# Kernel tuning notes

Hardware: AMD Instinct MI355X
Metric: run time of the kernel (lower is better)

Reference implementation:

```python
import jax, jax.numpy as jnp
import numpy as np

WINDOWP = 64
LN_EPS = 1e-5


def setup_inputs() -> dict:
    key = jax.random.key(0)
    ks = jax.random.split(key, 4)
    B, T, D = 8, 2048, 1024
    feature = jax.random.normal(ks[0], (B, T, D), dtype=jnp.float32)
    wq_w = jax.random.normal(ks[1], (D, D), dtype=jnp.float32) * 0.02  # x @ wq_w + wq_b
    wq_b = jnp.zeros((D,), dtype=jnp.float32)
    w2_w = jax.random.normal(ks[2], (D,), dtype=jnp.float32) * 0.02
    w2_b = jnp.zeros((1,), dtype=jnp.float32)
    ln_g = jnp.ones((D,), dtype=jnp.float32)
    ln_b = jnp.zeros((D,), dtype=jnp.float32)
    return {"feature": feature, "wq_w": wq_w, "wq_b": wq_b,
            "w2_w": w2_w, "w2_b": w2_b, "ln_g": ln_g, "ln_b": ln_b}


def _layer_norm(y, g, b):
    mu = jnp.mean(y, axis=-1, keepdims=True)
    var = jnp.mean((y - mu) ** 2, axis=-1, keepdims=True)
    return (y - mu) * jax.lax.rsqrt(var + LN_EPS) * g + b


def reference(feature, wq_w, wq_b, w2_w, w2_b, ln_g, ln_b):
    # feature: [B, T, D]
    B, T, D = feature.shape
    W = WINDOWP
    q_local = feature @ wq_w + wq_b  # [B, T, D]

    # First W positions: v_local[:, i] = feature[:, i]
    init_buf = feature[:, :W, :]  # sliding buffer of last W outputs, [B, W, D]

    def step(buf, q_i):
        # ki = v_local[:, i-W : i+1]; slot i is still zero when read (torch writes after)
        ki = jnp.concatenate([buf, jnp.zeros((B, 1, D), feature.dtype)], axis=1)  # [B, W+1, D]
        scores = jnp.einsum('bwd,d->bw', q_i[:, None, :] * ki, w2_w) + w2_b[0]  # [B, W+1]
        alpha = jax.nn.softmax(scores, axis=1)
        v_i = jnp.einsum('bwd,bw->bd', ki, alpha)  # [B, D]
        new_buf = jnp.concatenate([buf[:, 1:, :], v_i[:, None, :]], axis=1)
        return new_buf, v_i

    qs = jnp.transpose(q_local[:, W:, :], (1, 0, 2))  # [T-W, B, D]
    _, vs = jax.lax.scan(step, init_buf, qs)          # vs: [T-W, B, D]
    v_local = jnp.concatenate([feature[:, :W, :], jnp.transpose(vs, (1, 0, 2))], axis=1)

    y = jnp.tanh(v_local) * feature + feature
    return _layer_norm(y, ln_g, ln_b)
```

## Files before the change

### kernel.cpp

```cpp
#include <hip/hip_runtime.h>
#include <hip/hip_bf16.h>

#define B_ 8
#define T_ 2048
#define D_ 1024
#define W_ 64
#define LN_EPS 1e-5f
#define LOG2E 1.4426950408889634f

typedef __attribute__((ext_vector_type(8))) short bf16x8;
typedef __attribute__((ext_vector_type(4))) float f32x4;
typedef __attribute__((ext_vector_type(2))) float f32x2;
typedef unsigned short ushort_t;

__device__ __forceinline__ ushort_t f32_to_bf16(float f) {
    union { float ff; unsigned u; } c; c.ff = f;
    unsigned r = (c.u + 0x7fffu + ((c.u >> 16) & 1u)) >> 16;
    return (ushort_t)r;
}
__device__ __forceinline__ float bf16_to_f32(ushort_t h) {
    union { unsigned u; float f; } c; c.u = ((unsigned)h) << 16; return c.f;
}
__device__ __forceinline__ float tanh_fast(float x) {
    float xx = fminf(fmaxf(x, -20.f), 20.f);
    float e = __expf(2.f * xx);
    return 1.f - 2.f / (e + 1.f);
}
__device__ __forceinline__ float readlane_f(float v, int l) {
    return __int_as_float(__builtin_amdgcn_readlane(__float_as_int(v), l));
}
template <int CTRL>
__device__ __forceinline__ float dpp_add(float x) {
    int y = __builtin_amdgcn_update_dpp(0, __float_as_int(x), CTRL, 0xf, 0xf, true);
    return x + __int_as_float(y);
}
template <int CTRL>
__device__ __forceinline__ f32x2 pk_dpp_add(f32x2 v) {
    f32x2 t;
    t.x = __int_as_float(__builtin_amdgcn_update_dpp(0, __float_as_int(v.x), CTRL, 0xf, 0xf, true));
    t.y = __int_as_float(__builtin_amdgcn_update_dpp(0, __float_as_int(v.y), CTRL, 0xf, 0xf, true));
    return v + t;
}
__device__ __forceinline__ f32x2 sum64_pair(f32x2 v) {
    v = pk_dpp_add<0x111>(v);
    v = pk_dpp_add<0x112>(v);
    v = pk_dpp_add<0x114>(v);
    v = pk_dpp_add<0x118>(v);
    v = pk_dpp_add<0x142>(v);
    v = pk_dpp_add<0x143>(v);
    return v;
}
__device__ __forceinline__ float sum64_sc(float x) {
    x = dpp_add<0x111>(x);
    x = dpp_add<0x112>(x);
    x = dpp_add<0x114>(x);
    x = dpp_add<0x118>(x);
    x = dpp_add<0x142>(x);
    x = dpp_add<0x143>(x);
    return x;
}
__device__ __forceinline__ f32x2 lo2(f32x4 v) { return __builtin_shufflevector(v, v, 0, 1); }
__device__ __forceinline__ f32x2 hi2(f32x4 v) { return __builtin_shufflevector(v, v, 2, 3); }

__global__ void cvt_feat(const float* __restrict__ f, ushort_t* __restrict__ o, int n) {
    int i = blockIdx.x * blockDim.x + threadIdx.x;
    if (i < n) o[i] = f32_to_bf16(f[i]);
}

__global__ void cvt_wqT(const float* __restrict__ wq, ushort_t* __restrict__ o) {
    __shared__ float tile[64][65];
    int bi = blockIdx.x, bj = blockIdx.y, tid = threadIdx.x;
    int c = tid & 63, r4 = tid >> 6;
    for (int it = 0; it < 16; ++it) {
        int r = it * 4 + r4;
        tile[r][c] = wq[(size_t)(bi * 64 + r) * D_ + bj * 64 + c];
    }
    __syncthreads();
    for (int it = 0; it < 16; ++it) {
        int r = it * 4 + r4;
        o[(size_t)(bj * 64 + r) * D_ + bi * 64 + c] = f32_to_bf16(tile[c][r]);
    }
}

__global__ __launch_bounds__(256) void gemm_qw(
        const ushort_t* __restrict__ A, const ushort_t* __restrict__ BT,
        const float* __restrict__ wqb, const float* __restrict__ w2w,
        float* __restrict__ out) {
    const int K = 1024;
    __shared__ ushort_t Al[128][48];
    __shared__ ushort_t Bl[64][48];
    int tid = threadIdx.x;
    int lane = tid & 63, wv = tid >> 6;
    int wm = wv >> 1, wn = wv & 1;
    int m0 = blockIdx.x * 128, n0 = blockIdx.y * 64;
    int mrow = lane & 15, quad = lane >> 4;
    f32x4 acc[4][2] = {};
    for (int k0 = 0; k0 < K; k0 += 32) {
#pragma unroll
        for (int rep = 0; rep < 2; ++rep) {
            int idx = rep * 256 + tid;
            int r = idx >> 2, cp = (idx & 3) * 8;
            *(bf16x8*)&Al[r][cp] = *(const bf16x8*)&A[(size_t)(m0 + r) * K + k0 + cp];
        }
        {
            int r = tid >> 2, cp = (tid & 3) * 8;
            *(bf16x8*)&Bl[r][cp] = *(const bf16x8*)&BT[(size_t)(n0 + r) * K + k0 + cp];
        }
        __syncthreads();
        bf16x8 af[4], bfr[2];
#pragma unroll
        for (int ms = 0; ms < 4; ++ms) af[ms] = *(bf16x8*)&Al[wm * 64 + ms * 16 + mrow][quad * 8];
#pragma unroll
        for (int ns = 0; ns < 2; ++ns) bfr[ns] = *(bf16x8*)&Bl[wn * 32 + ns * 16 + mrow][quad * 8];
#pragma unroll
        for (int ms = 0; ms < 4; ++ms)
#pragma unroll
            for (int ns = 0; ns < 2; ++ns)
                acc[ms][ns] = __builtin_amdgcn_mfma_f32_16x16x32_bf16(af[ms], bfr[ns], acc[ms][ns], 0, 0, 0);
        __syncthreads();
    }
#pragma unroll
    for (int ns = 0; ns < 2; ++ns) {
        int n = n0 + wn * 32 + ns * 16 + mrow;
        float scale = w2w[n] * LOG2E, bias = wqb[n];
#pragma unroll
        for (int ms = 0; ms < 4; ++ms) {
#pragma unroll
            for (int r = 0; r < 4; ++r) {
                int m = m0 + wm * 64 + ms * 16 + quad * 4 + r;
                out[(size_t)m * D_ + n] = (acc[ms][ns][r] + bias) * scale;
            }
        }
    }
}

__global__ void featT_kernel(const float* __restrict__ feat, float* __restrict__ fT32,
                             ushort_t* __restrict__ fTh, ushort_t* __restrict__ fTl) {
    __shared__ float tile[64][65];
    int d0 = blockIdx.x * 64, b = blockIdx.y, tid = threadIdx.x;
    int c = tid & 63, r4 = tid >> 6;
#pragma unroll
    for (int it = 0; it < 16; ++it) {
        int r = it * 4 + r4;
        tile[r][c] = feat[((size_t)b * T_ + r) * D_ + d0 + c];
    }
    __syncthreads();
#pragma unroll
    for (int it = 0; it < 16; ++it) {
        int r = it * 4 + r4;
        float v = tile[c][r];
        size_t o = ((size_t)b * D_ + d0 + r) * 64 + c;
        fT32[o] = v;
        ushort_t h = f32_to_bf16(v);
        fTh[o] = h;
        fTl[o] = f32_to_bf16(v - bf16_to_f32(h));
    }
}

__global__ __launch_bounds__(256) void s0_gemm(
        const float* __restrict__ qw, const float* __restrict__ fT32,
        ushort_t* __restrict__ S0h, ushort_t* __restrict__ S0l) {
    __shared__ float As[64][17];
    __shared__ float Bs[16][65];
    int b = blockIdx.y;
    int t0 = 64 + blockIdx.x * 64;
    int tx = threadIdx.x & 15, ty = threadIdx.x >> 4;
    float acc[4][4] = {};
    for (int k0 = 0; k0 < D_; k0 += 16) {
#pragma unroll
        for (int i = 0; i < 4; ++i) {
            int idx = i * 256 + threadIdx.x;
            int r = idx >> 4, c = idx & 15;
            As[r][c] = qw[((size_t)b * T_ + t0 + r) * D_ + k0 + c];
        }
#pragma unroll
        for (int i = 0; i < 4; ++i) {
            int idx = i * 256 + threadIdx.x;
            int r = idx >> 6, c = idx & 63;
            Bs[r][c] = fT32[((size_t)b * D_ + k0 + r) * 64 + c];
        }
        __syncthreads();
#pragma unroll
        for (int kk = 0; kk < 16; ++kk)
#pragma unroll
            for (int i = 0; i < 4; ++i)
#pragma unroll
                for (int j = 0; j < 4; ++j)
                    acc[i][j] = fmaf(As[ty * 4 + i][kk], Bs[kk][tx * 4 + j], acc[i][j]);
        __syncthreads();
    }
#pragma unroll
    for (int i = 0; i < 4; ++i)
#pragma unroll
        for (int j = 0; j < 4; ++j) {
            float sc = acc[i][j];
            ushort_t h = f32_to_bf16(sc);
            size_t o = ((size_t)b * T_ + t0 + ty * 4 + i) * 64 + tx * 4 + j;
            S0h[o] = h;
            S0l[o] = f32_to_bf16(sc - bf16_to_f32(h));
        }
}

__global__ __launch_bounds__(64, 1) void core_kernel(
        const ushort_t* __restrict__ S0h, const ushort_t* __restrict__ S0l,
        float* __restrict__ gamma) {
    const int b = blockIdx.x;
    const int lane = threadIdx.x;
    const int n16 = lane & 15, quad = lane >> 4;
    __shared__ float ULDS[64 * 67];
    __shared__ __align__(16) float ALPH[64 * 68];
    __shared__ __align__(16) float B1L[16 * 68];
    __shared__ ushort_t CH[64 * 72];
    __shared__ ushort_t CL[64 * 72];
    __shared__ ushort_t CWTh[64 * 72];
    __shared__ ushort_t CWTl[64 * 72];

#pragma unroll
    for (int jj = 0; jj < 72; ++jj) {
        ushort_t idv = (jj == lane) ? (ushort_t)0x3F80 : (ushort_t)0;
        CH[lane * 72 + jj] = idv;  CL[lane * 72 + jj] = 0;
        CWTh[lane * 72 + jj] = idv; CWTl[lane * 72 + jj] = 0;
    }

#pragma unroll 1
    for (int p = 0; p < 31; ++p) {
        const int t0 = 64 + (p << 6);

        {
            bf16x8 Bh[4][2], Blo[4][2];
#pragma unroll
            for (int nt = 0; nt < 4; ++nt)
#pragma unroll
                for (int kt = 0; kt < 2; ++kt) {
                    int a = (nt * 16 + n16) * 72 + kt * 32 + quad * 8;
                    Bh[nt][kt] = *(const bf16x8*)&CH[a];
                    Blo[nt][kt] = *(const bf16x8*)&CL[a];
                }
#pragma unroll
            for (int mt = 0; mt < 4; ++mt) {
                bf16x8 Ah[2], Alo2[2];
#pragma unroll
                for (int kt = 0; kt < 2; ++kt) {
                    size_t a = ((size_t)b * T_ + t0 + mt * 16 + n16) * 64 + kt * 32 + quad * 8;
                    Ah[kt] = *(const bf16x8*)&S0h[a];
                    Alo2[kt] = *(const bf16x8*)&S0l[a];
                }
                f32x4 acc[4] = {};
#pragma unroll
                for (int nt = 0; nt < 4; ++nt)
#pragma unroll
                    for (int kt = 0; kt < 2; ++kt) {
                        acc[nt] = __builtin_amdgcn_mfma_f32_16x16x32_bf16(Ah[kt], Bh[nt][kt], acc[nt], 0, 0, 0);
                        acc[nt] = __builtin_amdgcn_mfma_f32_16x16x32_bf16(Ah[kt], Blo[nt][kt], acc[nt], 0, 0, 0);
                        acc[nt] = __builtin_amdgcn_mfma_f32_16x16x32_bf16(Alo2[kt], Bh[nt][kt], acc[nt], 0, 0, 0);
                    }
#pragma unroll
                for (int nt = 0; nt < 4; ++nt)
#pragma unroll
                    for (int r = 0; r < 4; ++r)
                        ULDS[(mt * 16 + quad * 4 + r) * 67 + nt * 16 + n16] = acc[nt][r];
            }
        }

        f32x2 Xa2[8], Xb2[8], Xc2[8], Xd2[8];
#pragma unroll
        for (int l2 = 0; l2 < 8; ++l2) {
            Xa2[l2].x = ULDS[lane * 67 + 2 * l2];
            Xa2[l2].y = ULDS[lane * 67 + 2 * l2 + 1];
            Xb2[l2].x = ULDS[lane * 67 + 16 + 2 * l2];
            Xb2[l2].y = ULDS[lane * 67 + 16 + 2 * l2 + 1];
            Xc2[l2].x = ULDS[lane * 67 + 32 + 2 * l2];
            Xc2[l2].y = ULDS[lane * 67 + 32 + 2 * l2 + 1];
            Xd2[l2].x = ULDS[lane * 67 + 48 + 2 * l2];
            Xd2[l2].y = ULDS[lane * 67 + 48 + 2 * l2 + 1];
        }
        float row = ULDS[lane];
        float nxt = ULDS[67 + lane];

#pragma unroll 1
        for (int j = 0; j < 4; ++j) {
#pragma unroll
            for (int sl = 0; sl < 16; ++sl) {
                const int s = (j << 4) | sl;
                float nxt2v = 0.f;
                if (s <= 61) nxt2v = ULDS[(s + 2) * 67 + lane];
                float e = __builtin_amdgcn_exp2f(row);
                ALPH[s * 68 + lane] = e;
                f32x4 A[16];
                if (s < 63) {
#pragma unroll
                    for (int i = 0; i < 16; ++i)
                        A[i] = *(const f32x4*)&ALPH[s * 68 + i * 4];
                }
                f32x2 v; v.x = e; v.y = e * nxt;
                v = sum64_pair(v);
                float w = 0.f;
                if (s <= 61) w = sum64_sc(e * nxt2v);
                float tot = readlane_f(v.x, 63) + 1.f;
                float cs  = readlane_f(v.y, 63);
                float r = __builtin_amdgcn_rcpf(tot);
                if (s < 63) {
                    float u_next = cs * r;
                    row = (lane == s) ? u_next : nxt;
                    if (s <= 61) {
                        float u_next2 = readlane_f(w, 63) * r;
                        nxt = (lane == s) ? u_next2 : nxt2v;
                    } else {
                        nxt = 0.f;
                    }
                    f32x2 acc0 = {0.f, 0.f}, acc1 = {0.f, 0.f}, acc2 = {0.f, 0.f}, acc3 = {0.f, 0.f};
#pragma unroll
                    for (int i2 = 0; i2 < 4; ++i2) {
                        f32x4 aa = A[i2];
                        acc0 = __builtin_elementwise_fma(lo2(aa), Xa2[2 * i2], acc0);
                        acc1 = __builtin_elementwise_fma(hi2(aa), Xa2[2 * i2 + 1], acc1);
                        f32x4 ab = A[4 + i2];
                        acc2 = __builtin_elementwise_fma(lo2(ab), Xb2[2 * i2], acc2);
                        acc3 = __builtin_elementwise_fma(hi2(ab), Xb2[2 * i2 + 1], acc3);
                        f32x4 ac = A[8 + i2];
                        acc0 = __builtin_elementwise_fma(lo2(ac), Xc2[2 * i2], acc0);
                        acc1 = __builtin_elementwise_fma(hi2(ac), Xc2[2 * i2 + 1], acc1);
                        f32x4 ad = A[12 + i2];
                        acc2 = __builtin_elementwise_fma(lo2(ad), Xd2[2 * i2], acc2);
                        acc3 = __builtin_elementwise_fma(hi2(ad), Xd2[2 * i2 + 1], acc3);
                    }
                    f32x2 u2 = (acc0 + acc1) + (acc2 + acc3);
                    float u_new = (u2.x + u2.y) * r;
                    if (j == 0)      { if (sl & 1) Xa2[sl >> 1].y = u_new; else Xa2[sl >> 1].x = u_new; }
                    else if (j == 1) { if (sl & 1) Xb2[sl >> 1].y = u_new; else Xb2[sl >> 1].x = u_new; }
                    else if (j == 2) { if (sl & 1) Xc2[sl >> 1].y = u_new; else Xc2[sl >> 1].x = u_new; }
                    else             { if (sl & 1) Xd2[sl >> 1].y = u_new; else Xd2[sl >> 1].x = u_new; }
                    if (lane > s) ULDS[lane * 67 + s] = u_new;
                }
                if (lane == 0) ALPH[s * 68 + 64] = r;
            }

            {
                const int J0 = j << 4;
                float rrow = ALPH[(J0 + n16) * 68 + 64];
                bf16x8 Aah[2], Aal[2];
#pragma unroll
                for (int kt = 0; kt < 2; ++kt) {
                    float v[8];
                    *(float4*)&v[0] = *(const float4*)&ALPH[(J0 + n16) * 68 + kt * 32 + quad * 8];
                    *(float4*)&v[4] = *(const float4*)&ALPH[(J0 + n16) * 68 + kt * 32 + quad * 8 + 4];
                    bf16x8 h, l;
#pragma unroll
                    for (int i = 0; i < 8; ++i) {
                        float val = v[i] * rrow;
                        ushort_t hh = f32_to_bf16(val);
                        h[i] = (short)hh;
                        l[i] = (short)f32_to_bf16(val - bf16_to_f32(hh));
                    }
                    Aah[kt] = h; Aal[kt] = l;
                }
#pragma unroll
                for (int nt = 0; nt < 4; ++nt) {
                    f32x4 a = {};
#pragma unroll
                    for (int kt = 0; kt < 2; ++kt) {
                        bf16x8 bh = *(const bf16x8*)&CWTh[(nt * 16 + n16) * 72 + kt * 32 + quad * 8];
                        bf16x8 bl = *(const bf16x8*)&CWTl[(nt * 16 + n16) * 72 + kt * 32 + quad * 8];
                        a = __builtin_amdgcn_mfma_f32_16x16x32_bf16(Aah[kt], bh, a, 0, 0, 0);
                        a = __builtin_amdgcn_mfma_f32_16x16x32_bf16(Aah[kt], bl, a, 0, 0, 0);
                        a = __builtin_amdgcn_mfma_f32_16x16x32_bf16(Aal[kt], bh, a, 0, 0, 0);
                    }
#pragma unroll
                    for (int r = 0; r < 4; ++r)
                        B1L[(quad * 4 + r) * 68 + nt * 16 + n16] = a[r];
                }
                float D[16];
#pragma unroll
                for (int sl = 0; sl < 16; ++sl) {
                    float corr = 0.f;
                    const float* arow = &ALPH[(J0 + sl) * 68 + J0];
#pragma unroll
                    for (int c = 0; c < 4; ++c) {
                        if (sl > 4 * c) {
                            float4 am = *(const float4*)&arow[4 * c];
                            if (sl > 4 * c + 0) corr = fmaf(am.x, D[4 * c + 0], corr);
                            if (sl > 4 * c + 1) corr = fmaf(am.y, D[4 * c + 1], corr);
                            if (sl > 4 * c + 2) corr = fmaf(am.z, D[4 * c + 2], corr);
                            if (sl > 4 * c + 3) corr = fmaf(am.w, D[4 * c + 3], corr);
                        }
                    }
                    float rsl = ALPH[(J0 + sl) * 68 + 64];
                    float g = fmaf(rsl, corr, B1L[sl * 68 + lane]);
                    const int slot = J0 + sl;
                    float oldv = bf16_to_f32(CH[slot * 72 + lane]) + bf16_to_f32(CL[slot * 72 + lane]);
                    D[sl] = g - oldv;
                    gamma[((size_t)b * T_ + t0 + slot) * 64 + lane] = g;
                    ushort_t gh = f32_to_bf16(g);
                    ushort_t gl2 = f32_to_bf16(g - bf16_to_f32(gh));
                    CH[slot * 72 + lane] = gh;  CL[slot * 72 + lane] = gl2;
                    CWTh[lane * 72 + slot] = gh; CWTl[lane * 72 + slot] = gl2;
                }
            }
        }
    }
}

__global__ __launch_bounds__(256) void prologue_kernel(
        const float* __restrict__ feat, float* __restrict__ out,
        const float* __restrict__ lng, const float* __restrict__ lnb) {
    int b = blockIdx.y, t = blockIdx.x, tid = threadIdx.x;
    __shared__ float red[4][2];
    size_t base = ((size_t)b * T_ + t) * D_;
    float4 f4 = *(const float4*)&feat[base + tid * 4];
    float4 y;
    y.x = tanh_fast(f4.x) * f4.x + f4.x;
    y.y = tanh_fast(f4.y) * f4.y + f4.y;
    y.z = tanh_fast(f4.z) * f4.z + f4.z;
    y.w = tanh_fast(f4.w) * f4.w + f4.w;
    float s1 = y.x + y.y + y.z + y.w;
    float s2 = y.x * y.x + y.y * y.y + y.z * y.z + y.w * y.w;
#pragma unroll
    for (int m = 1; m < 64; m <<= 1) { s1 += __shfl_xor(s1, m, 64); s2 += __shfl_xor(s2, m, 64); }
    if ((tid & 63) == 0) { red[tid >> 6][0] = s1; red[tid >> 6][1] = s2; }
    __syncthreads();
    float mu = (red[0][0] + red[1][0] + red[2][0] + red[3][0]) * (1.f / D_);
    float m2 = (red[0][1] + red[1][1] + red[2][1] + red[3][1]) * (1.f / D_);
    float rv = rsqrtf(fmaxf(m2 - mu * mu, 0.f) + LN_EPS);
    float4 g4 = *(const float4*)&lng[tid * 4];
    float4 b4 = *(const float4*)&lnb[tid * 4];
    float4 o;
    o.x = (y.x - mu) * rv * g4.x + b4.x;
    o.y = (y.y - mu) * rv * g4.y + b4.y;
    o.z = (y.z - mu) * rv * g4.z + b4.z;
    o.w = (y.w - mu) * rv * g4.w + b4.w;
    *(float4*)&out[base + tid * 4] = o;
}

__global__ __launch_bounds__(256) void final_kernel(
        const float* __restrict__ gamma, const ushort_t* __restrict__ fTh,
        const ushort_t* __restrict__ fTl, const float* __restrict__ feat,
        const float* __restrict__ lng, const float* __restrict__ lnb,
        float* __restrict__ out) {
    const int b = blockIdx.y;
    const int t0 = 64 + blockIdx.x * 16;
    const int tid = threadIdx.x, lane = tid & 63, wv = tid >> 6;
    const int n16 = lane & 15, quad = lane >> 4;
    __shared__ float wsum[4][16][2];
    __shared__ float lnp[16][2];

    bf16x8 Ah[2], Alo[2];
    {
        const float* gr = &gamma[((size_t)b * T_ + t0 + n16) * 64];
#pragma unroll
        for (int kt = 0; kt < 2; ++kt) {
            float g[8];
            *(float4*)&g[0] = *(const float4*)&gr[kt * 32 + quad * 8];
            *(float4*)&g[4] = *(const float4*)&gr[kt * 32 + quad * 8 + 4];
            bf16x8 h, l;
#pragma unroll
            for (int i = 0; i < 8; ++i) {
                ushort_t hh = f32_to_bf16(g[i]);
                h[i] = (short)hh;
                l[i] = (short)f32_to_bf16(g[i] - bf16_to_f32(hh));
            }
            Ah[kt] = h; Alo[kt] = l;
        }
    }
    f32x4 acc[16];
#pragma unroll
    for (int j = 0; j < 16; ++j) {
        const int d = wv * 256 + j * 16 + n16;
        const ushort_t* fr = &fTh[((size_t)b * D_ + d) * 64];
        const ushort_t* fr2 = &fTl[((size_t)b * D_ + d) * 64];
        f32x4 a = {0.f, 0.f, 0.f, 0.f};
#pragma unroll
        for (int kt = 0; kt < 2; ++kt) {
            bf16x8 bh = *(const bf16x8*)&fr[kt * 32 + quad * 8];
            bf16x8 bl = *(const bf16x8*)&fr2[kt * 32 + quad * 8];
            a = __builtin_amdgcn_mfma_f32_16x16x32_bf16(Ah[kt], bh, a, 0, 0, 0);
            a = __builtin_amdgcn_mfma_f32_16x16x32_bf16(Ah[kt], bl, a, 0, 0, 0);
            a = __builtin_amdgcn_mfma_f32_16x16x32_bf16(Alo[kt], bh, a, 0, 0, 0);
        }
        acc[j] = a;
    }
    float s1[4] = {0.f, 0.f, 0.f, 0.f}, s2[4] = {0.f, 0.f, 0.f, 0.f};
#pragma unroll
    for (int j = 0; j < 16; ++j) {
        const int d = wv * 256 + j * 16 + n16;
#pragma unroll
        for (int r = 0; r < 4; ++r) {
            float f = feat[((size_t)b * T_ + t0 + quad * 4 + r) * D_ + d];
            float y = tanh_fast(acc[j][r]) * f + f;
            acc[j][r] = y;
            s1[r] += y;
            s2[r] += y * y;
        }
    }
#pragma unroll
    for (int m = 1; m < 16; m <<= 1)
#pragma unroll
        for (int r = 0; r < 4; ++r) { s1[r] += __shfl_xor(s1[r], m, 64); s2[r] += __shfl_xor(s2[r], m, 64); }
    if (n16 == 0) {
#pragma unroll
        for (int r = 0; r < 4; ++r) { wsum[wv][quad * 4 + r][0] = s1[r]; wsum[wv][quad * 4 + r][1] = s2[r]; }
    }
    __syncthreads();
    if (tid < 16) {
        float a = 0.f, c = 0.f;
#pragma unroll
        for (int w2 = 0; w2 < 4; ++w2) { a += wsum[w2][tid][0]; c += wsum[w2][tid][1]; }
        float mu = a * (1.f / D_);
        float var = c * (1.f / D_) - mu * mu;
        lnp[tid][0] = mu;
        lnp[tid][1] = rsqrtf(fmaxf(var, 0.f) + LN_EPS);
    }
    __syncthreads();
#pragma unroll
    for (int j = 0; j < 16; ++j) {
        const int d = wv * 256 + j * 16 + n16;
        float gd = lng[d], bd = lnb[d];
#pragma unroll
        for (int r = 0; r < 4; ++r) {
            int row = quad * 4 + r;
            out[((size_t)b * T_ + t0 + row) * D_ + d] = (acc[j][r] - lnp[row][0]) * lnp[row][1] * gd + bd;
        }
    }
}

extern "C" void kernel_launch(void* const* d_in, const int* in_sizes, int n_in,
                              void* d_out, int out_size, void* d_ws, size_t ws_size,
                              hipStream_t stream) {
    const float* feature = (const float*)d_in[0];
    const float* wq_w    = (const float*)d_in[1];
    const float* wq_b    = (const float*)d_in[2];
    const float* w2_w    = (const float*)d_in[3];
    const float* ln_g    = (const float*)d_in[5];
    const float* ln_b    = (const float*)d_in[6];
    float* out = (float*)d_out;

    uint8_t* ws = (uint8_t*)d_ws;
    ushort_t* featbf = (ushort_t*)(ws);
    ushort_t* wqT    = (ushort_t*)(ws + 32u * 1024 * 1024);
    float*    gamma = (float*)(ws);
    ushort_t* S0h   = (ushort_t*)(ws + 4u * 1024 * 1024);
    ushort_t* S0l   = (ushort_t*)(ws + 6u * 1024 * 1024);
    float*    fT32  = (float*)(ws + 8u * 1024 * 1024);
    ushort_t* fTh   = (ushort_t*)(ws + 10u * 1024 * 1024);
    ushort_t* fTl   = (ushort_t*)(ws + 11u * 1024 * 1024);

    const int ntot = B_ * T_ * D_;
    cvt_feat<<<(ntot + 255) / 256, 256, 0, stream>>>(feature, featbf, ntot);
    cvt_wqT<<<dim3(16, 16), 256, 0, stream>>>(wq_w, wqT);
    gemm_qw<<<dim3(128, 16), 256, 0, stream>>>(featbf, wqT, wq_b, w2_w, out);
    featT_kernel<<<dim3(16, 8), 256, 0, stream>>>(feature, fT32, fTh, fTl);
    s0_gemm<<<dim3(31, 8), 256, 0, stream>>>(out, fT32, S0h, S0l);
    core_kernel<<<8, 64, 0, stream>>>(S0h, S0l, gamma);
    prologue_kernel<<<dim3(64, 8), 256, 0, stream>>>(feature, out, ln_g, ln_b);
    final_kernel<<<dim3(124, 8), 256, 0, stream>>>(gamma, fTh, fTl, feature, ln_g, ln_b, out);
}
```

Baseline: 1.400 ms.

## Software-pipeline serial softmax recurrence by deferring update dot product one step

Restructures the inner serial step loop so that the dot product producing the previous step's update (scaled by the previous reciprocal) runs before the current step's reductions. A readlane-based correction term fixes the next-row prediction that depends on the just-produced value. The loop-carried ALPH row load moves to the end of the step, with a special reload after each 16-step block. The goal is to shorten the critical dependency chain per step. It also hoists the S0 global loads ahead of the MFMA loop, and replaces the ALPH-based correction in the block update with register readlanes plus preloaded B1L, old values and reciprocals. The price is more registers and more complex boundary logic, which could introduce errors at block edges.

Result: no change. 1.424 ms (+1.7%).

```diff
diff --git a/kernel.cpp b/kernel.cpp
--- a/kernel.cpp
+++ b/kernel.cpp
@@ -222,6 +222,9 @@
         CWTh[lane * 72 + jj] = idv; CWTl[lane * 72 + jj] = 0;
     }
 
+    f32x4 A[16];
+    float r_prev = 0.f;
+
 #pragma unroll 1
     for (int p = 0; p < 31; ++p) {
         const int t0 = 64 + (p << 6);
@@ -236,23 +239,25 @@
                     Bh[nt][kt] = *(const bf16x8*)&CH[a];
                     Blo[nt][kt] = *(const bf16x8*)&CL[a];
                 }
-#pragma unroll
-            for (int mt = 0; mt < 4; ++mt) {
-                bf16x8 Ah[2], Alo2[2];
+            bf16x8 SAh[4][2], SAl[4][2];
+#pragma unroll
+            for (int mt = 0; mt < 4; ++mt)
 #pragma unroll
                 for (int kt = 0; kt < 2; ++kt) {
                     size_t a = ((size_t)b * T_ + t0 + mt * 16 + n16) * 64 + kt * 32 + quad * 8;
-                    Ah[kt] = *(const bf16x8*)&S0h[a];
-                    Alo2[kt] = *(const bf16x8*)&S0l[a];
-                }
+                    SAh[mt][kt] = *(const bf16x8*)&S0h[a];
+                    SAl[mt][kt] = *(const bf16x8*)&S0l[a];
+                }
+#pragma unroll
+            for (int mt = 0; mt < 4; ++mt) {
                 f32x4 acc[4] = {};
 #pragma unroll
                 for (int nt = 0; nt < 4; ++nt)
 #pragma unroll
                     for (int kt = 0; kt < 2; ++kt) {
-                        acc[nt] = __builtin_amdgcn_mfma_f32_16x16x32_bf16(Ah[kt], Bh[nt][kt], acc[nt], 0, 0, 0);
-                        acc[nt] = __builtin_amdgcn_mfma_f32_16x16x32_bf16(Ah[kt], Blo[nt][kt], acc[nt], 0, 0, 0);
-                        acc[nt] = __builtin_amdgcn_mfma_f32_16x16x32_bf16(Alo2[kt], Bh[nt][kt], acc[nt], 0, 0, 0);
+                        acc[nt] = __builtin_amdgcn_mfma_f32_16x16x32_bf16(SAh[mt][kt], Bh[nt][kt], acc[nt], 0, 0, 0);
+                        acc[nt] = __builtin_amdgcn_mfma_f32_16x16x32_bf16(SAh[mt][kt], Blo[nt][kt], acc[nt], 0, 0, 0);
+                        acc[nt] = __builtin_amdgcn_mfma_f32_16x16x32_bf16(SAl[mt][kt], Bh[nt][kt], acc[nt], 0, 0, 0);
                     }
 #pragma unroll
                 for (int nt = 0; nt < 4; ++nt)
@@ -276,6 +281,7 @@
         }
         float row = ULDS[lane];
         float nxt = ULDS[67 + lane];
+        float Esave[16];
 
 #pragma unroll 1
         for (int j = 0; j < 4; ++j) {
@@ -285,29 +291,9 @@
                 float nxt2v = 0.f;
                 if (s <= 61) nxt2v = ULDS[(s + 2) * 67 + lane];
                 float e = __builtin_amdgcn_exp2f(row);
-                ALPH[s * 68 + lane] = e;
-                f32x4 A[16];
-                if (s < 63) {
-#pragma unroll
-                    for (int i = 0; i < 16; ++i)
-                        A[i] = *(const f32x4*)&ALPH[s * 68 + i * 4];
-                }
-                f32x2 v; v.x = e; v.y = e * nxt;
-                v = sum64_pair(v);
-                float w = 0.f;
-                if (s <= 61) w = sum64_sc(e * nxt2v);
-                float tot = readlane_f(v.x, 63) + 1.f;
-                float cs  = readlane_f(v.y, 63);
-                float r = __builtin_amdgcn_rcpf(tot);
-                if (s < 63) {
-                    float u_next = cs * r;
-                    row = (lane == s) ? u_next : nxt;
-                    if (s <= 61) {
-                        float u_next2 = readlane_f(w, 63) * r;
-                        nxt = (lane == s) ? u_next2 : nxt2v;
-                    } else {
-                        nxt = 0.f;
-                    }
+                Esave[sl] = e;
+                float u_new = 0.f;
+                if (s >= 1 && s <= 61) {
                     f32x2 acc0 = {0.f, 0.f}, acc1 = {0.f, 0.f}, acc2 = {0.f, 0.f}, acc3 = {0.f, 0.f};
 #pragma unroll
                     for (int i2 = 0; i2 < 4; ++i2) {
@@ -325,14 +311,50 @@
                         acc3 = __builtin_elementwise_fma(hi2(ad), Xd2[2 * i2 + 1], acc3);
                     }
                     f32x2 u2 = (acc0 + acc1) + (acc2 + acc3);
-                    float u_new = (u2.x + u2.y) * r;
-                    if (j == 0)      { if (sl & 1) Xa2[sl >> 1].y = u_new; else Xa2[sl >> 1].x = u_new; }
-                    else if (j == 1) { if (sl & 1) Xb2[sl >> 1].y = u_new; else Xb2[sl >> 1].x = u_new; }
-                    else if (j == 2) { if (sl & 1) Xc2[sl >> 1].y = u_new; else Xc2[sl >> 1].x = u_new; }
-                    else             { if (sl & 1) Xd2[sl >> 1].y = u_new; else Xd2[sl >> 1].x = u_new; }
-                    if (lane > s) ULDS[lane * 67 + s] = u_new;
+                    u_new = (u2.x + u2.y) * r_prev;
+                    if (sl >= 1) {
+                        const int c = sl - 1;
+                        if (j == 0)      { if (c & 1) Xa2[c >> 1].y = u_new; else Xa2[c >> 1].x = u_new; }
+                        else if (j == 1) { if (c & 1) Xb2[c >> 1].y = u_new; else Xb2[c >> 1].x = u_new; }
+                        else if (j == 2) { if (c & 1) Xc2[c >> 1].y = u_new; else Xc2[c >> 1].x = u_new; }
+                        else             { if (c & 1) Xd2[c >> 1].y = u_new; else Xd2[c >> 1].x = u_new; }
+                    } else {
+                        if (j == 1)      Xa2[7].y = u_new;
+                        else if (j == 2) Xb2[7].y = u_new;
+                        else             Xc2[7].y = u_new;
+                    }
+                    if (lane > s - 1) ULDS[lane * 67 + (s - 1)] = u_new;
+                }
+                ALPH[s * 68 + lane] = e;
+                if (s <= 60 && sl != 15) {
+#pragma unroll
+                    for (int i = 0; i < 16; ++i)
+                        A[i] = *(const f32x4*)&ALPH[s * 68 + i * 4];
+                }
+                f32x2 v; v.x = e; v.y = e * nxt;
+                v = sum64_pair(v);
+                float w_ = 0.f;
+                if (s <= 61) w_ = sum64_sc(e * nxt2v);
+                float tot = readlane_f(v.x, 63) + 1.f;
+                float cs  = readlane_f(v.y, 63);
+                float r = __builtin_amdgcn_rcpf(tot);
+                if (s < 63) {
+                    row = (lane == s) ? cs * r : nxt;
+                    if (s <= 61) {
+                        float wfix = readlane_f(w_, 63);
+                        float nn = nxt2v;
+                        if (s >= 1) {
+                            float cnew = readlane_f(u_new, s + 2);
+                            wfix += readlane_f(e, s - 1) * (cnew - readlane_f(nxt2v, s - 1));
+                            nn = (lane == s - 1) ? cnew : nn;
+                        }
+                        nxt = (lane == s) ? wfix * r : nn;
+                    } else {
+                        nxt = 0.f;
+                    }
                 }
                 if (lane == 0) ALPH[s * 68 + 64] = r;
+                r_prev = r;
             }
 
             {
@@ -369,32 +391,36 @@
                     for (int r = 0; r < 4; ++r)
                         B1L[(quad * 4 + r) * 68 + nt * 16 + n16] = a[r];
                 }
+                float b1v[16], ov[16], rr[16];
+#pragma unroll
+                for (int s2 = 0; s2 < 16; ++s2) {
+                    b1v[s2] = B1L[s2 * 68 + lane];
+                    ov[s2] = bf16_to_f32(CH[(J0 + s2) * 72 + lane]) + bf16_to_f32(CL[(J0 + s2) * 72 + lane]);
+                    rr[s2] = ALPH[(J0 + s2) * 68 + 64];
+                }
                 float D[16];
 #pragma unroll
-                for (int sl = 0; sl < 16; ++sl) {
+                for (int s2 = 0; s2 < 16; ++s2) {
                     float corr = 0.f;
-                    const float* arow = &ALPH[(J0 + sl) * 68 + J0];
-#pragma unroll
-                    for (int c = 0; c < 4; ++c) {
-                        if (sl > 4 * c) {
-                            float4 am = *(const float4*)&arow[4 * c];
-                            if (sl > 4 * c + 0) corr = fmaf(am.x, D[4 * c + 0], corr);
-                            if (sl > 4 * c + 1) corr = fmaf(am.y, D[4 * c + 1], corr);
-                            if (sl > 4 * c + 2) corr = fmaf(am.z, D[4 * c + 2], corr);
-                            if (sl > 4 * c + 3) corr = fmaf(am.w, D[4 * c + 3], corr);
-                        }
-                    }
-                    float rsl = ALPH[(J0 + sl) * 68 + 64];
-                    float g = fmaf(rsl, corr, B1L[sl * 68 + lane]);
-                    const int slot = J0 + sl;
-                    float oldv = bf16_to_f32(CH[slot * 72 + lane]) + bf16_to_f32(CL[slot * 72 + lane]);
-                    D[sl] = g - oldv;
+#pragma unroll
+                    for (int c = 0; c < 16; ++c)
+                        if (c < s2)
+                            corr = fmaf(readlane_f(Esave[s2], J0 + c), D[c], corr);
+                    float g = fmaf(rr[s2], corr, b1v[s2]);
+                    const int slot = J0 + s2;
+                    D[s2] = g - ov[s2];
                     gamma[((size_t)b * T_ + t0 + slot) * 64 + lane] = g;
                     ushort_t gh = f32_to_bf16(g);
                     ushort_t gl2 = f32_to_bf16(g - bf16_to_f32(gh));
                     CH[slot * 72 + lane] = gh;  CL[slot * 72 + lane] = gl2;
                     CWTh[lane * 72 + slot] = gh; CWTl[lane * 72 + slot] = gl2;
                 }
+            }
+            if (j < 3) {
+                const int s15 = (j << 4) | 15;
+#pragma unroll
+                for (int i = 0; i < 16; ++i)
+                    A[i] = *(const f32x4*)&ALPH[s15 * 68 + i * 4];
             }
         }
     }
```
